# Kernel optimization log

Measured on AMD Instinct MI355X. Metric: run time of the kernel, lower is better.

Reference implementation:

```python
import jax, jax.numpy as jnp
import numpy as np

N = 1000   # node count forced by fc1_1 in_features=1680 (see shape derivation)
E = 8000   # edges, avg degree ~8
F_IN = 6   # node feature dim (first 3 = pos, zeroed in forward)


def setup_inputs() -> dict:
    key = jax.random.key(0)
    ks = jax.random.split(key, 24)
    f = lambda k, s, sc=1.0: jax.random.normal(k, s, dtype=jnp.float32) * sc
    inp = {
        "x": f(ks[0], (N, F_IN)),
        "edge_index": jax.random.randint(ks[1], (2, E), 0, N, dtype=jnp.int64),
        # GCNConv weights (xavier-ish scale)
        "W1": f(ks[2], (F_IN, 32), 0.4), "b1": jnp.zeros((32,), jnp.float32),
        "W2": f(ks[3], (32, 32), 0.18), "b2": jnp.zeros((32,), jnp.float32),
        # Conv2d kernels, OIHW
        "k1": f(ks[4], (3, 1, 3, 2), 0.3), "kb1": jnp.zeros((3,), jnp.float32),
        "k2": f(ks[5], (6, 3, 3, 2), 0.2), "kb2": jnp.zeros((6,), jnp.float32),
        "k3": f(ks[6], (3, 6, 3, 2), 0.2), "kb3": jnp.zeros((3,), jnp.float32),
        "k4": f(ks[7], (1, 3, 3, 2), 0.2), "kb4": jnp.zeros((1,), jnp.float32),
        # FC head (torch Linear layout: [out, in])
        "fw1": f(ks[8], (1024, 1680), 0.02), "fb1": jnp.zeros((1024,), jnp.float32),
        "fw2": f(ks[9], (1024, 1024), 0.03), "fb2": jnp.zeros((1024,), jnp.float32),
        "fw3": f(ks[10], (64, 1024), 0.03), "fb3": jnp.zeros((64,), jnp.float32),
    }
    return inp


def _conv2d(x, w, b):
    out = jax.lax.conv_general_dilated(
        x, w, window_strides=(1, 1), padding="VALID",
        dimension_numbers=("NCHW", "OIHW", "NCHW"))
    return out + b[None, :, None, None]


def _maxpool2(x):  # MaxPool2d((2,1), stride=(2,1))
    return jax.lax.reduce_window(x, -jnp.inf, jax.lax.max,
                                 (1, 1, 2, 1), (1, 1, 2, 1), "VALID")


def reference(x, edge_index, W1, b1, W2, b2, k1, kb1, k2, kb2, k3, kb3, k4, kb4,
              fw1, fb1, fw2, fb2, fw3, fb3):
    num_nodes = x.shape[0]
    # forward zeroes the first 3 features (positions)
    x = x.at[:, :3].set(0.0)

    loop = jnp.arange(num_nodes)
    row = jnp.concatenate([edge_index[0], loop])
    col = jnp.concatenate([edge_index[1], loop])
    deg = jnp.zeros((num_nodes,), x.dtype).at[col].add(1.0)
    dinv = jnp.where(deg > 0, jax.lax.rsqrt(deg), 0.0)
    norm = (dinv[row] * dinv[col])[:, None]  # [E+N, 1]

    def gcn(h, W, b):
        hw = h @ W                                   # [N, 32]
        msg = hw[row] * norm                         # gather + scale
        return jax.ops.segment_sum(msg, col, num_segments=num_nodes) + b

    leaky = lambda v: jnp.where(v > 0, v, 0.2 * v)   # LeakyReLU(0.2)
    h = leaky(gcn(x, W1, b1))
    h = leaky(gcn(h, W2, b2))                        # [N, 32]

    img = h[None, None]                              # [1, 1, N, 32]
    img = _maxpool2(jax.nn.relu(_conv2d(img, k1, kb1)))   # [1,3,499,31]
    img = _maxpool2(jax.nn.relu(_conv2d(img, k2, kb2)))   # [1,6,248,30]
    img = _maxpool2(jax.nn.relu(_conv2d(img, k3, kb3)))   # [1,3,123,29]
    img = _maxpool2(jax.nn.relu(_conv2d(img, k4, kb4)))   # [1,1,60,28]

    v = img.reshape(-1)                              # [1680]
    v = v @ fw1.T + fb1                              # no activation between FCs (as in source)
    v = v @ fw2.T + fb2
    v = v @ fw3.T + fb3                              # [64]
    return v
```

## Files before the change

kernel.cpp:

```cpp
#include <hip/hip_runtime.h>

#define LEAKY(v) ((v) > 0.0f ? (v) : 0.2f * (v))

__global__ void k1_prep(const float* __restrict__ x, const int* __restrict__ col,
                        const float* __restrict__ W1, float* __restrict__ deg,
                        float* __restrict__ aggs ,
                        float* __restrict__ xw, int n, int E) {
    int tid = blockIdx.x * blockDim.x + threadIdx.x;
    int NT = gridDim.x * blockDim.x;
    for (int i = tid; i < 2 * n * 32; i += NT) aggs[i] = 0.0f;
    for (int e = tid; e < E; e += NT) atomicAdd(&deg[col[e]], 1.0f);
    for (int t = tid; t < n * 32; t += NT) {
        int j = t & 31, nn = t >> 5;
        xw[t] = x[nn*6+3] * W1[96+j]
              + x[nn*6+4] * W1[128+j]
              + x[nn*6+5] * W1[160+j];
    }
}

__global__ void k_scatter(const float* __restrict__ xw, const float* __restrict__ deg,
                          const int* __restrict__ row, const int* __restrict__ col,
                          float* __restrict__ agg, int E, int n) {
    int tid = blockIdx.x * blockDim.x + threadIdx.x;
    int total = (E + n) * 32;
    if (tid >= total) return;
    int e = tid >> 5, j = tid & 31;
    int r, c; float nrm;
    if (e < E) {
        r = row[e]; c = col[e];
        nrm = (1.0f / sqrtf(deg[r] + 1.0f)) * (1.0f / sqrtf(deg[c] + 1.0f));
    } else {
        r = c = e - E;
        nrm = 1.0f / (deg[r] + 1.0f);
    }
    atomicAdd(&agg[c * 32 + j], xw[r * 32 + j] * nrm);
}

__global__ void k3_xw2(const float* __restrict__ agg1, const float* __restrict__ b1,
                       const float* __restrict__ W2, float* __restrict__ xw, int n) {
    int tid = blockIdx.x * blockDim.x + threadIdx.x;
    if (tid >= n * 32) return;
    int j = tid & 31, nn = tid >> 5;
    const float* a = agg1 + nn * 32;
    float s = 0.0f;
#pragma unroll
    for (int f = 0; f < 32; ++f) {
        float v = a[f] + b1[f];
        v = LEAKY(v);
        s += v * W2[f * 32 + j];
    }
    xw[tid] = s;
}

__global__ void k5_conv1(const float* __restrict__ h2, const float* __restrict__ b2,
                         const float* __restrict__ w, const float* __restrict__ bias,
                         float* __restrict__ out) {
    const int Hp = 499, Wo = 31, total = 3 * Hp * Wo;
    int t0 = blockIdx.x * blockDim.x + threadIdx.x;
    if (t0 >= total) return;
    int ow = t0 % Wo; int t = t0 / Wo; int oh = t % Hp; int co = t / Hp;
    const float* ip = h2 + (2 * oh) * 32 + ow;
    float vals[4][2];
#pragma unroll
    for (int r = 0; r < 4; ++r)
#pragma unroll
        for (int cx = 0; cx < 2; ++cx) {
            float v = ip[r * 32 + cx] + b2[ow + cx];
            vals[r][cx] = LEAKY(v);
        }
    const float* wp = w + co * 6;
    float a0 = vals[0][0]*wp[0] + vals[0][1]*wp[1] + vals[1][0]*wp[2]
             + vals[1][1]*wp[3] + vals[2][0]*wp[4] + vals[2][1]*wp[5];
    float a1 = vals[1][0]*wp[0] + vals[1][1]*wp[1] + vals[2][0]*wp[2]
             + vals[2][1]*wp[3] + vals[3][0]*wp[4] + vals[3][1]*wp[5];
    float m = fmaxf(a0, a1) + bias[co];
    out[t0] = fmaxf(m, 0.0f);
}

__global__ void k6_conv2(const float* __restrict__ in, const float* __restrict__ w,
                         const float* __restrict__ bias, float* __restrict__ out) {
    const int CI = 3, Hin = 499, Win = 31, Hp = 248, Wo = 30, total = 6 * Hp * Wo;
    int t0 = blockIdx.x * blockDim.x + threadIdx.x;
    if (t0 >= total) return;
    int ow = t0 % Wo; int t = t0 / Wo; int oh = t % Hp; int co = t / Hp;
    float a0 = 0.0f, a1 = 0.0f;
#pragma unroll
    for (int ci = 0; ci < CI; ++ci) {
        const float* q = in + (ci * Hin + 2 * oh) * Win + ow;
        const float* wp = w + (co * CI + ci) * 6;
        float r00 = q[0],     r01 = q[1];
        float r10 = q[Win],   r11 = q[Win+1];
        float r20 = q[2*Win], r21 = q[2*Win+1];
        float r30 = q[3*Win], r31 = q[3*Win+1];
        a0 += r00*wp[0] + r01*wp[1] + r10*wp[2] + r11*wp[3] + r20*wp[4] + r21*wp[5];
        a1 += r10*wp[0] + r11*wp[1] + r20*wp[2] + r21*wp[3] + r30*wp[4] + r31*wp[5];
    }
    float m = fmaxf(a0, a1) + bias[co];
    out[t0] = fmaxf(m, 0.0f);
}

__global__ void k7_conv3(const float* __restrict__ in, const float* __restrict__ w,
                         const float* __restrict__ bias, float* __restrict__ out) {
    const int CI = 6, Hin = 248, Win = 30, Hp = 123, Wo = 29, total = 3 * Hp * Wo;
    int t0 = blockIdx.x * blockDim.x + threadIdx.x;
    if (t0 >= total) return;
    int ow = t0 % Wo; int t = t0 / Wo; int oh = t % Hp; int co = t / Hp;
    float a0 = 0.0f, a1 = 0.0f;
#pragma unroll
    for (int ci = 0; ci < CI; ++ci) {
        const float* q = in + (ci * Hin + 2 * oh) * Win + ow;
        const float* wp = w + (co * CI + ci) * 6;
        float r00 = q[0],     r01 = q[1];
        float r10 = q[Win],   r11 = q[Win+1];
        float r20 = q[2*Win], r21 = q[2*Win+1];
        float r30 = q[3*Win], r31 = q[3*Win+1];
        a0 += r00*wp[0] + r01*wp[1] + r10*wp[2] + r11*wp[3] + r20*wp[4] + r21*wp[5];
        a1 += r10*wp[0] + r11*wp[1] + r20*wp[2] + r21*wp[3] + r30*wp[4] + r31*wp[5];
    }
    float m = fmaxf(a0, a1) + bias[co];
    out[t0] = fmaxf(m, 0.0f);
}

__global__ __launch_bounds__(256) void k8_conv4_fc1(
        const float* __restrict__ c3, const float* __restrict__ k4,
        const float* __restrict__ kb4, const float* __restrict__ fw1,
        const float* __restrict__ fb1, float* __restrict__ f1) {
    __shared__ __align__(16) float lc4[1680];
    const int Hin = 123, Win = 29, Wo = 28;
    float kb = kb4[0];
    for (int t0 = (int)threadIdx.x; t0 < 1680; t0 += 256) {
        int ow = t0 % Wo; int oh = t0 / Wo;
        float a0 = 0.0f, a1 = 0.0f;
#pragma unroll
        for (int ci = 0; ci < 3; ++ci) {
            const float* q = c3 + (ci * Hin + 2 * oh) * Win + ow;
            const float* wp = k4 + ci * 6;
            float r00 = q[0],     r01 = q[1];
            float r10 = q[Win],   r11 = q[Win+1];
            float r20 = q[2*Win], r21 = q[2*Win+1];
            float r30 = q[3*Win], r31 = q[3*Win+1];
            a0 += r00*wp[0] + r01*wp[1] + r10*wp[2] + r11*wp[3] + r20*wp[4] + r21*wp[5];
            a1 += r10*wp[0] + r11*wp[1] + r20*wp[2] + r21*wp[3] + r30*wp[4] + r31*wp[5];
        }
        float m = fmaxf(a0, a1) + kb;
        lc4[t0] = fmaxf(m, 0.0f);
    }
    __syncthreads();
    int wv = threadIdx.x >> 6, lane = threadIdx.x & 63;
    int o = blockIdx.x * 4 + wv;
    const float4* wr = (const float4*)(fw1 + (size_t)o * 1680);
    const float4* vv = (const float4*)lc4;
    float s = 0.0f;
    for (int i = lane; i < 420; i += 64) {
        float4 a = vv[i], ww = wr[i];
        s += a.x*ww.x + a.y*ww.y + a.z*ww.z + a.w*ww.w;
    }
#pragma unroll
    for (int off = 32; off > 0; off >>= 1) s += __shfl_down(s, off, 64);
    if (lane == 0) f1[o] = s + fb1[o];
}

__global__ __launch_bounds__(256) void k_fc1024(const float* __restrict__ v,
                                                const float* __restrict__ w,
                                                const float* __restrict__ b,
                                                float* __restrict__ out) {
    int wv = threadIdx.x >> 6, lane = threadIdx.x & 63;
    int o = blockIdx.x * 4 + wv;
    const float4* wr = (const float4*)(w + (size_t)o * 1024);
    const float4* vv = (const float4*)v;
    float s = 0.0f;
#pragma unroll
    for (int i = 0; i < 4; ++i) {
        float4 a = vv[lane + 64*i], ww = wr[lane + 64*i];
        s += a.x*ww.x + a.y*ww.y + a.z*ww.z + a.w*ww.w;
    }
#pragma unroll
    for (int off = 32; off > 0; off >>= 1) s += __shfl_down(s, off, 64);
    if (lane == 0) out[o] = s + b[o];
}

extern "C" void kernel_launch(void* const* d_in, const int* in_sizes, int n_in,
                              void* d_out, int out_size, void* d_ws, size_t ws_size,
                              hipStream_t stream) {
    const float* x   = (const float*)d_in[0];
    const int*   ei  = (const int*)d_in[1];
    const float* W1  = (const float*)d_in[2];
    const float* b1  = (const float*)d_in[3];
    const float* W2  = (const float*)d_in[4];
    const float* b2  = (const float*)d_in[5];
    const float* k1  = (const float*)d_in[6];
    const float* kb1 = (const float*)d_in[7];
    const float* k2  = (const float*)d_in[8];
    const float* kb2 = (const float*)d_in[9];
    const float* k3  = (const float*)d_in[10];
    const float* kb3 = (const float*)d_in[11];
    const float* k4  = (const float*)d_in[12];
    const float* kb4 = (const float*)d_in[13];
    const float* fw1 = (const float*)d_in[14];
    const float* fb1 = (const float*)d_in[15];
    const float* fw2 = (const float*)d_in[16];
    const float* fb2 = (const float*)d_in[17];
    const float* fw3 = (const float*)d_in[18];
    const float* fb3 = (const float*)d_in[19];

    int n = in_sizes[0] / 6;
    int E = in_sizes[1] / 2;
    const int* row = ei;
    const int* col = ei + E;

    float* ws   = (float*)d_ws;
    float* deg  = ws;
    float* agg1 = ws + 1024;
    float* agg2 = agg1 + 32000;
    float* xw   = agg2 + 32000;
    float* c1   = xw + 32000;
    float* c2   = c1 + 46407;
    float* c3   = c2 + 44640;
    float* f1   = c3 + 10704;
    float* f2   = f1 + 1024;

    const int B = 256;

    hipMemsetAsync(deg, 0, n * sizeof(float), stream);
    k1_prep<<<256, B, 0, stream>>>(x, col, W1, deg, agg1, xw, n, E);
    int st = (E + n) * 32;
    k_scatter<<<(st + B - 1) / B, B, 0, stream>>>(xw, deg, row, col, agg1, E, n);
    k3_xw2<<<(n * 32 + B - 1) / B, B, 0, stream>>>(agg1, b1, W2, xw, n);
    k_scatter<<<(st + B - 1) / B, B, 0, stream>>>(xw, deg, row, col, agg2, E, n);
    k5_conv1<<<(3 * 499 * 31 + B - 1) / B, B, 0, stream>>>(agg2, b2, k1, kb1, c1);
    k6_conv2<<<(6 * 248 * 30 + B - 1) / B, B, 0, stream>>>(c1, k2, kb2, c2);
    k7_conv3<<<(3 * 123 * 29 + B - 1) / B, B, 0, stream>>>(c2, k3, kb3, c3);
    k8_conv4_fc1<<<256, B, 0, stream>>>(c3, k4, kb4, fw1, fb1, f1);
    k_fc1024<<<256, B, 0, stream>>>(f1, fw2, fb2, f2);
    k_fc1024<<<16, B, 0, stream>>>(f2, fw3, fb3, (float*)d_out);
}
```

Measured before the change: 136.0 us.

## Fuse all stages into one cooperative persistent kernel with grid syncs

Replaces the memset plus nine separate kernel launches with a single cooperative kernel of 256 blocks that runs every stage in grid-stride loops, separated by grid.sync barriers. The aim is to remove per-launch overhead and inter-kernel gaps, which likely dominate at this small problem size. In exchange, the scatter and conv stages that previously used many blocks now run on only 256 blocks, and each grid-wide barrier has its own cost. Zeroing of deg and agg buffers also moves inside the kernel.

```diff
diff --git a/kernel.cpp b/kernel.cpp
--- a/kernel.cpp
+++ b/kernel.cpp
@@ -1,236 +1,276 @@
 #include <hip/hip_runtime.h>
+#include <hip/hip_cooperative_groups.h>
+
+namespace cg = cooperative_groups;
 
 #define LEAKY(v) ((v) > 0.0f ? (v) : 0.2f * (v))
 
-__global__ void k1_prep(const float* __restrict__ x, const int* __restrict__ col,
-                        const float* __restrict__ W1, float* __restrict__ deg,
-                        float* __restrict__ aggs ,
-                        float* __restrict__ xw, int n, int E) {
-    int tid = blockIdx.x * blockDim.x + threadIdx.x;
-    int NT = gridDim.x * blockDim.x;
-    for (int i = tid; i < 2 * n * 32; i += NT) aggs[i] = 0.0f;
-    for (int e = tid; e < E; e += NT) atomicAdd(&deg[col[e]], 1.0f);
-    for (int t = tid; t < n * 32; t += NT) {
+struct Params {
+    const float* x;  const int* row; const int* col;
+    const float* W1; const float* b1; const float* W2; const float* b2;
+    const float* k1; const float* kb1; const float* k2; const float* kb2;
+    const float* k3; const float* kb3; const float* k4; const float* kb4;
+    const float* fw1; const float* fb1; const float* fw2; const float* fb2;
+    const float* fw3; const float* fb3;
+    float* deg;
+    float* agg1;
+    float* agg2;
+    float* xw;
+    float* c1;
+    float* c2;
+    float* c3;
+    float* f1;
+    float* f2;
+    float* out;
+    int n; int E;
+};
+
+__global__ __launch_bounds__(256) void fused_all(Params p) {
+    cg::grid_group grid = cg::this_grid();
+    const int T  = blockIdx.x * 256 + (int)threadIdx.x;
+    const int NT = gridDim.x * 256;
+    __shared__ __align__(16) float lc4[1680];
+
+    for (int i = T; i < 1024 + 64000; i += NT) p.deg[i] = 0.0f;
+    grid.sync();
+
+    for (int e = T; e < p.E; e += NT) atomicAdd(&p.deg[p.col[e]], 1.0f);
+    for (int t = T; t < p.n * 32; t += NT) {
         int j = t & 31, nn = t >> 5;
-        xw[t] = x[nn*6+3] * W1[96+j]
-              + x[nn*6+4] * W1[128+j]
-              + x[nn*6+5] * W1[160+j];
-    }
-}
-
-__global__ void k_scatter(const float* __restrict__ xw, const float* __restrict__ deg,
-                          const int* __restrict__ row, const int* __restrict__ col,
-                          float* __restrict__ agg, int E, int n) {
-    int tid = blockIdx.x * blockDim.x + threadIdx.x;
-    int total = (E + n) * 32;
-    if (tid >= total) return;
-    int e = tid >> 5, j = tid & 31;
-    int r, c; float nrm;
-    if (e < E) {
-        r = row[e]; c = col[e];
-        nrm = (1.0f / sqrtf(deg[r] + 1.0f)) * (1.0f / sqrtf(deg[c] + 1.0f));
-    } else {
-        r = c = e - E;
-        nrm = 1.0f / (deg[r] + 1.0f);
-    }
-    atomicAdd(&agg[c * 32 + j], xw[r * 32 + j] * nrm);
-}
-
-__global__ void k3_xw2(const float* __restrict__ agg1, const float* __restrict__ b1,
-                       const float* __restrict__ W2, float* __restrict__ xw, int n) {
-    int tid = blockIdx.x * blockDim.x + threadIdx.x;
-    if (tid >= n * 32) return;
-    int j = tid & 31, nn = tid >> 5;
-    const float* a = agg1 + nn * 32;
-    float s = 0.0f;
-#pragma unroll
-    for (int f = 0; f < 32; ++f) {
-        float v = a[f] + b1[f];
-        v = LEAKY(v);
-        s += v * W2[f * 32 + j];
-    }
-    xw[tid] = s;
-}
-
-__global__ void k5_conv1(const float* __restrict__ h2, const float* __restrict__ b2,
-                         const float* __restrict__ w, const float* __restrict__ bias,
-                         float* __restrict__ out) {
-    const int Hp = 499, Wo = 31, total = 3 * Hp * Wo;
-    int t0 = blockIdx.x * blockDim.x + threadIdx.x;
-    if (t0 >= total) return;
-    int ow = t0 % Wo; int t = t0 / Wo; int oh = t % Hp; int co = t / Hp;
-    const float* ip = h2 + (2 * oh) * 32 + ow;
-    float vals[4][2];
-#pragma unroll
-    for (int r = 0; r < 4; ++r)
-#pragma unroll
-        for (int cx = 0; cx < 2; ++cx) {
-            float v = ip[r * 32 + cx] + b2[ow + cx];
-            vals[r][cx] = LEAKY(v);
-        }
-    const float* wp = w + co * 6;
-    float a0 = vals[0][0]*wp[0] + vals[0][1]*wp[1] + vals[1][0]*wp[2]
-             + vals[1][1]*wp[3] + vals[2][0]*wp[4] + vals[2][1]*wp[5];
-    float a1 = vals[1][0]*wp[0] + vals[1][1]*wp[1] + vals[2][0]*wp[2]
-             + vals[2][1]*wp[3] + vals[3][0]*wp[4] + vals[3][1]*wp[5];
-    float m = fmaxf(a0, a1) + bias[co];
-    out[t0] = fmaxf(m, 0.0f);
-}
-
-__global__ void k6_conv2(const float* __restrict__ in, const float* __restrict__ w,
-                         const float* __restrict__ bias, float* __restrict__ out) {
-    const int CI = 3, Hin = 499, Win = 31, Hp = 248, Wo = 30, total = 6 * Hp * Wo;
-    int t0 = blockIdx.x * blockDim.x + threadIdx.x;
-    if (t0 >= total) return;
-    int ow = t0 % Wo; int t = t0 / Wo; int oh = t % Hp; int co = t / Hp;
-    float a0 = 0.0f, a1 = 0.0f;
-#pragma unroll
-    for (int ci = 0; ci < CI; ++ci) {
-        const float* q = in + (ci * Hin + 2 * oh) * Win + ow;
-        const float* wp = w + (co * CI + ci) * 6;
-        float r00 = q[0],     r01 = q[1];
-        float r10 = q[Win],   r11 = q[Win+1];
-        float r20 = q[2*Win], r21 = q[2*Win+1];
-        float r30 = q[3*Win], r31 = q[3*Win+1];
-        a0 += r00*wp[0] + r01*wp[1] + r10*wp[2] + r11*wp[3] + r20*wp[4] + r21*wp[5];
-        a1 += r10*wp[0] + r11*wp[1] + r20*wp[2] + r21*wp[3] + r30*wp[4] + r31*wp[5];
-    }
-    float m = fmaxf(a0, a1) + bias[co];
-    out[t0] = fmaxf(m, 0.0f);
-}
-
-__global__ void k7_conv3(const float* __restrict__ in, const float* __restrict__ w,
-                         const float* __restrict__ bias, float* __restrict__ out) {
-    const int CI = 6, Hin = 248, Win = 30, Hp = 123, Wo = 29, total = 3 * Hp * Wo;
-    int t0 = blockIdx.x * blockDim.x + threadIdx.x;
-    if (t0 >= total) return;
-    int ow = t0 % Wo; int t = t0 / Wo; int oh = t % Hp; int co = t / Hp;
-    float a0 = 0.0f, a1 = 0.0f;
-#pragma unroll
-    for (int ci = 0; ci < CI; ++ci) {
-        const float* q = in + (ci * Hin + 2 * oh) * Win + ow;
-        const float* wp = w + (co * CI + ci) * 6;
-        float r00 = q[0],     r01 = q[1];
-        float r10 = q[Win],   r11 = q[Win+1];
-        float r20 = q[2*Win], r21 = q[2*Win+1];
-        float r30 = q[3*Win], r31 = q[3*Win+1];
-        a0 += r00*wp[0] + r01*wp[1] + r10*wp[2] + r11*wp[3] + r20*wp[4] + r21*wp[5];
-        a1 += r10*wp[0] + r11*wp[1] + r20*wp[2] + r21*wp[3] + r30*wp[4] + r31*wp[5];
-    }
-    float m = fmaxf(a0, a1) + bias[co];
-    out[t0] = fmaxf(m, 0.0f);
-}
-
-__global__ __launch_bounds__(256) void k8_conv4_fc1(
-        const float* __restrict__ c3, const float* __restrict__ k4,
-        const float* __restrict__ kb4, const float* __restrict__ fw1,
-        const float* __restrict__ fb1, float* __restrict__ f1) {
-    __shared__ __align__(16) float lc4[1680];
-    const int Hin = 123, Win = 29, Wo = 28;
-    float kb = kb4[0];
-    for (int t0 = (int)threadIdx.x; t0 < 1680; t0 += 256) {
-        int ow = t0 % Wo; int oh = t0 / Wo;
-        float a0 = 0.0f, a1 = 0.0f;
-#pragma unroll
-        for (int ci = 0; ci < 3; ++ci) {
-            const float* q = c3 + (ci * Hin + 2 * oh) * Win + ow;
-            const float* wp = k4 + ci * 6;
-            float r00 = q[0],     r01 = q[1];
-            float r10 = q[Win],   r11 = q[Win+1];
-            float r20 = q[2*Win], r21 = q[2*Win+1];
-            float r30 = q[3*Win], r31 = q[3*Win+1];
-            a0 += r00*wp[0] + r01*wp[1] + r10*wp[2] + r11*wp[3] + r20*wp[4] + r21*wp[5];
-            a1 += r10*wp[0] + r11*wp[1] + r20*wp[2] + r21*wp[3] + r30*wp[4] + r31*wp[5];
-        }
-        float m = fmaxf(a0, a1) + kb;
-        lc4[t0] = fmaxf(m, 0.0f);
-    }
-    __syncthreads();
-    int wv = threadIdx.x >> 6, lane = threadIdx.x & 63;
-    int o = blockIdx.x * 4 + wv;
-    const float4* wr = (const float4*)(fw1 + (size_t)o * 1680);
-    const float4* vv = (const float4*)lc4;
-    float s = 0.0f;
-    for (int i = lane; i < 420; i += 64) {
-        float4 a = vv[i], ww = wr[i];
-        s += a.x*ww.x + a.y*ww.y + a.z*ww.z + a.w*ww.w;
-    }
-#pragma unroll
-    for (int off = 32; off > 0; off >>= 1) s += __shfl_down(s, off, 64);
-    if (lane == 0) f1[o] = s + fb1[o];
-}
-
-__global__ __launch_bounds__(256) void k_fc1024(const float* __restrict__ v,
-                                                const float* __restrict__ w,
-                                                const float* __restrict__ b,
-                                                float* __restrict__ out) {
-    int wv = threadIdx.x >> 6, lane = threadIdx.x & 63;
-    int o = blockIdx.x * 4 + wv;
-    const float4* wr = (const float4*)(w + (size_t)o * 1024);
-    const float4* vv = (const float4*)v;
-    float s = 0.0f;
-#pragma unroll
-    for (int i = 0; i < 4; ++i) {
-        float4 a = vv[lane + 64*i], ww = wr[lane + 64*i];
-        s += a.x*ww.x + a.y*ww.y + a.z*ww.z + a.w*ww.w;
-    }
-#pragma unroll
-    for (int off = 32; off > 0; off >>= 1) s += __shfl_down(s, off, 64);
-    if (lane == 0) out[o] = s + b[o];
+        p.xw[t] = p.x[nn*6+3] * p.W1[96+j]
+                + p.x[nn*6+4] * p.W1[128+j]
+                + p.x[nn*6+5] * p.W1[160+j];
+    }
+    grid.sync();
+
+    {
+        const int total = (p.E + p.n) * 32;
+        for (int t = T; t < total; t += NT) {
+            int e = t >> 5, j = t & 31;
+            int r, c; float nrm;
+            if (e < p.E) {
+                r = p.row[e]; c = p.col[e];
+                nrm = (1.0f / sqrtf(p.deg[r] + 1.0f)) * (1.0f / sqrtf(p.deg[c] + 1.0f));
+            } else {
+                r = c = e - p.E;
+                nrm = 1.0f / (p.deg[r] + 1.0f);
+            }
+            atomicAdd(&p.agg1[c * 32 + j], p.xw[r * 32 + j] * nrm);
+        }
+    }
+    grid.sync();
+
+    for (int t = T; t < p.n * 32; t += NT) {
+        int j = t & 31, nn = t >> 5;
+        const float* a = p.agg1 + nn * 32;
+        float s = 0.0f;
+#pragma unroll
+        for (int f = 0; f < 32; ++f) {
+            float v = a[f] + p.b1[f];
+            v = LEAKY(v);
+            s += v * p.W2[f * 32 + j];
+        }
+        p.xw[t] = s;
+    }
+    grid.sync();
+
+    {
+        const int total = (p.E + p.n) * 32;
+        for (int t = T; t < total; t += NT) {
+            int e = t >> 5, j = t & 31;
+            int r, c; float nrm;
+            if (e < p.E) {
+                r = p.row[e]; c = p.col[e];
+                nrm = (1.0f / sqrtf(p.deg[r] + 1.0f)) * (1.0f / sqrtf(p.deg[c] + 1.0f));
+            } else {
+                r = c = e - p.E;
+                nrm = 1.0f / (p.deg[r] + 1.0f);
+            }
+            atomicAdd(&p.agg2[c * 32 + j], p.xw[r * 32 + j] * nrm);
+        }
+    }
+    grid.sync();
+
+    {
+        const int Hp = 499, Wo = 31, total = 3 * Hp * Wo;
+        for (int t0 = T; t0 < total; t0 += NT) {
+            int ow = t0 % Wo; int t = t0 / Wo; int oh = t % Hp; int co = t / Hp;
+            const float* ip = p.agg2 + (2 * oh) * 32 + ow;
+            float vals[4][2];
+#pragma unroll
+            for (int r = 0; r < 4; ++r)
+#pragma unroll
+                for (int cx = 0; cx < 2; ++cx) {
+                    float v = ip[r * 32 + cx] + p.b2[ow + cx];
+                    vals[r][cx] = LEAKY(v);
+                }
+            const float* wp = p.k1 + co * 6;
+            float a0 = vals[0][0]*wp[0] + vals[0][1]*wp[1] + vals[1][0]*wp[2]
+                     + vals[1][1]*wp[3] + vals[2][0]*wp[4] + vals[2][1]*wp[5];
+            float a1 = vals[1][0]*wp[0] + vals[1][1]*wp[1] + vals[2][0]*wp[2]
+                     + vals[2][1]*wp[3] + vals[3][0]*wp[4] + vals[3][1]*wp[5];
+            float m = fmaxf(a0, a1) + p.kb1[co];
+            p.c1[t0] = fmaxf(m, 0.0f);
+        }
+    }
+    grid.sync();
+
+    {
+        const int CI = 3, Hin = 499, Win = 31, Hp = 248, Wo = 30, total = 6 * Hp * Wo;
+        for (int t0 = T; t0 < total; t0 += NT) {
+            int ow = t0 % Wo; int t = t0 / Wo; int oh = t % Hp; int co = t / Hp;
+            float a0 = 0.0f, a1 = 0.0f;
+#pragma unroll
+            for (int ci = 0; ci < CI; ++ci) {
+                const float* q = p.c1 + (ci * Hin + 2 * oh) * Win + ow;
+                const float* wp = p.k2 + (co * CI + ci) * 6;
+                float r00 = q[0],     r01 = q[1];
+                float r10 = q[Win],   r11 = q[Win+1];
+                float r20 = q[2*Win], r21 = q[2*Win+1];
+                float r30 = q[3*Win], r31 = q[3*Win+1];
+                a0 += r00*wp[0] + r01*wp[1] + r10*wp[2] + r11*wp[3] + r20*wp[4] + r21*wp[5];
+                a1 += r10*wp[0] + r11*wp[1] + r20*wp[2] + r21*wp[3] + r30*wp[4] + r31*wp[5];
+            }
+            float m = fmaxf(a0, a1) + p.kb2[co];
+            p.c2[t0] = fmaxf(m, 0.0f);
+        }
+    }
+    grid.sync();
+
+    {
+        const int CI = 6, Hin = 248, Win = 30, Hp = 123, Wo = 29, total = 3 * Hp * Wo;
+        for (int t0 = T; t0 < total; t0 += NT) {
+            int ow = t0 % Wo; int t = t0 / Wo; int oh = t % Hp; int co = t / Hp;
+            float a0 = 0.0f, a1 = 0.0f;
+#pragma unroll
+            for (int ci = 0; ci < CI; ++ci) {
+                const float* q = p.c2 + (ci * Hin + 2 * oh) * Win + ow;
+                const float* wp = p.k3 + (co * CI + ci) * 6;
+                float r00 = q[0],     r01 = q[1];
+                float r10 = q[Win],   r11 = q[Win+1];
+                float r20 = q[2*Win], r21 = q[2*Win+1];
+                float r30 = q[3*Win], r31 = q[3*Win+1];
+                a0 += r00*wp[0] + r01*wp[1] + r10*wp[2] + r11*wp[3] + r20*wp[4] + r21*wp[5];
+                a1 += r10*wp[0] + r11*wp[1] + r20*wp[2] + r21*wp[3] + r30*wp[4] + r31*wp[5];
+            }
+            float m = fmaxf(a0, a1) + p.kb3[co];
+            p.c3[t0] = fmaxf(m, 0.0f);
+        }
+    }
+    grid.sync();
+
+    {
+        const int Hin = 123, Win = 29, Wo = 28;
+        float kb = p.kb4[0];
+        for (int t0 = (int)threadIdx.x; t0 < 1680; t0 += 256) {
+            int ow = t0 % Wo; int oh = t0 / Wo;
+            float a0 = 0.0f, a1 = 0.0f;
+#pragma unroll
+            for (int ci = 0; ci < 3; ++ci) {
+                const float* q = p.c3 + (ci * Hin + 2 * oh) * Win + ow;
+                const float* wp = p.k4 + ci * 6;
+                float r00 = q[0],     r01 = q[1];
+                float r10 = q[Win],   r11 = q[Win+1];
+                float r20 = q[2*Win], r21 = q[2*Win+1];
+                float r30 = q[3*Win], r31 = q[3*Win+1];
+                a0 += r00*wp[0] + r01*wp[1] + r10*wp[2] + r11*wp[3] + r20*wp[4] + r21*wp[5];
+                a1 += r10*wp[0] + r11*wp[1] + r20*wp[2] + r21*wp[3] + r30*wp[4] + r31*wp[5];
+            }
+            float m = fmaxf(a0, a1) + kb;
+            lc4[t0] = fmaxf(m, 0.0f);
+        }
+        __syncthreads();
+        int wv = (int)threadIdx.x >> 6, lane = (int)threadIdx.x & 63;
+        int o = blockIdx.x * 4 + wv;
+        const float4* wr = (const float4*)(p.fw1 + (size_t)o * 1680);
+        const float4* vv = (const float4*)lc4;
+        float s = 0.0f;
+        for (int i = lane; i < 420; i += 64) {
+            float4 a = vv[i], ww = wr[i];
+            s += a.x*ww.x + a.y*ww.y + a.z*ww.z + a.w*ww.w;
+        }
+#pragma unroll
+        for (int off = 32; off > 0; off >>= 1) s += __shfl_down(s, off, 64);
+        if (lane == 0) p.f1[o] = s + p.fb1[o];
+    }
+    grid.sync();
+
+    {
+        int wv = (int)threadIdx.x >> 6, lane = (int)threadIdx.x & 63;
+        int o = blockIdx.x * 4 + wv;
+        const float4* wr = (const float4*)(p.fw2 + (size_t)o * 1024);
+        const float4* vv = (const float4*)p.f1;
+        float s = 0.0f;
+#pragma unroll
+        for (int i = 0; i < 4; ++i) {
+            float4 a = vv[lane + 64*i], ww = wr[lane + 64*i];
+            s += a.x*ww.x + a.y*ww.y + a.z*ww.z + a.w*ww.w;
+        }
+#pragma unroll
+        for (int off = 32; off > 0; off >>= 1) s += __shfl_down(s, off, 64);
+        if (lane == 0) p.f2[o] = s + p.fb2[o];
+    }
+    grid.sync();
+
+    if (blockIdx.x < 16) {
+        int wv = (int)threadIdx.x >> 6, lane = (int)threadIdx.x & 63;
+        int o = blockIdx.x * 4 + wv;
+        const float4* wr = (const float4*)(p.fw3 + (size_t)o * 1024);
+        const float4* vv = (const float4*)p.f2;
+        float s = 0.0f;
+#pragma unroll
+        for (int i = 0; i < 4; ++i) {
+            float4 a = vv[lane + 64*i], ww = wr[lane + 64*i];
+            s += a.x*ww.x + a.y*ww.y + a.z*ww.z + a.w*ww.w;
+        }
+#pragma unroll
+        for (int off = 32; off > 0; off >>= 1) s += __shfl_down(s, off, 64);
+        if (lane == 0) p.out[o] = s + p.fb3[o];
+    }
 }
 
 extern "C" void kernel_launch(void* const* d_in, const int* in_sizes, int n_in,
                               void* d_out, int out_size, void* d_ws, size_t ws_size,
                               hipStream_t stream) {
-    const float* x   = (const float*)d_in[0];
-    const int*   ei  = (const int*)d_in[1];
-    const float* W1  = (const float*)d_in[2];
-    const float* b1  = (const float*)d_in[3];
-    const float* W2  = (const float*)d_in[4];
-    const float* b2  = (const float*)d_in[5];
-    const float* k1  = (const float*)d_in[6];
-    const float* kb1 = (const float*)d_in[7];
-    const float* k2  = (const float*)d_in[8];
-    const float* kb2 = (const float*)d_in[9];
-    const float* k3  = (const float*)d_in[10];
-    const float* kb3 = (const float*)d_in[11];
-    const float* k4  = (const float*)d_in[12];
-    const float* kb4 = (const float*)d_in[13];
-    const float* fw1 = (const float*)d_in[14];
-    const float* fb1 = (const float*)d_in[15];
-    const float* fw2 = (const float*)d_in[16];
-    const float* fb2 = (const float*)d_in[17];
-    const float* fw3 = (const float*)d_in[18];
-    const float* fb3 = (const float*)d_in[19];
-
-    int n = in_sizes[0] / 6;
-    int E = in_sizes[1] / 2;
-    const int* row = ei;
-    const int* col = ei + E;
-
-    float* ws   = (float*)d_ws;
-    float* deg  = ws;
-    float* agg1 = ws + 1024;
-    float* agg2 = agg1 + 32000;
-    float* xw   = agg2 + 32000;
-    float* c1   = xw + 32000;
-    float* c2   = c1 + 46407;
-    float* c3   = c2 + 44640;
-    float* f1   = c3 + 10704;
-    float* f2   = f1 + 1024;
-
-    const int B = 256;
-
-    hipMemsetAsync(deg, 0, n * sizeof(float), stream);
-    k1_prep<<<256, B, 0, stream>>>(x, col, W1, deg, agg1, xw, n, E);
-    int st = (E + n) * 32;
-    k_scatter<<<(st + B - 1) / B, B, 0, stream>>>(xw, deg, row, col, agg1, E, n);
-    k3_xw2<<<(n * 32 + B - 1) / B, B, 0, stream>>>(agg1, b1, W2, xw, n);
-    k_scatter<<<(st + B - 1) / B, B, 0, stream>>>(xw, deg, row, col, agg2, E, n);
-    k5_conv1<<<(3 * 499 * 31 + B - 1) / B, B, 0, stream>>>(agg2, b2, k1, kb1, c1);
-    k6_conv2<<<(6 * 248 * 30 + B - 1) / B, B, 0, stream>>>(c1, k2, kb2, c2);
-    k7_conv3<<<(3 * 123 * 29 + B - 1) / B, B, 0, stream>>>(c2, k3, kb3, c3);
-    k8_conv4_fc1<<<256, B, 0, stream>>>(c3, k4, kb4, fw1, fb1, f1);
-    k_fc1024<<<256, B, 0, stream>>>(f1, fw2, fb2, f2);
-    k_fc1024<<<16, B, 0, stream>>>(f2, fw3, fb3, (float*)d_out);
+    Params hp;
+    hp.x   = (const float*)d_in[0];
+    const int* ei = (const int*)d_in[1];
+    hp.W1  = (const float*)d_in[2];
+    hp.b1  = (const float*)d_in[3];
+    hp.W2  = (const float*)d_in[4];
+    hp.b2  = (const float*)d_in[5];
+    hp.k1  = (const float*)d_in[6];
+    hp.kb1 = (const float*)d_in[7];
+    hp.k2  = (const float*)d_in[8];
+    hp.kb2 = (const float*)d_in[9];
+    hp.k3  = (const float*)d_in[10];
+    hp.kb3 = (const float*)d_in[11];
+    hp.k4  = (const float*)d_in[12];
+    hp.kb4 = (const float*)d_in[13];
+    hp.fw1 = (const float*)d_in[14];
+    hp.fb1 = (const float*)d_in[15];
+    hp.fw2 = (const float*)d_in[16];
+    hp.fb2 = (const float*)d_in[17];
+    hp.fw3 = (const float*)d_in[18];
+    hp.fb3 = (const float*)d_in[19];
+
+    hp.n = in_sizes[0] / 6;
+    hp.E = in_sizes[1] / 2;
+    hp.row = ei;
+    hp.col = ei + hp.E;
+
+    float* ws = (float*)d_ws;
+    hp.deg  = ws;
+    hp.agg1 = ws + 1024;
+    hp.agg2 = hp.agg1 + 32000;
+    hp.xw   = hp.agg2 + 32000;
+    hp.c1   = hp.xw + 32000;
+    hp.c2   = hp.c1 + 46408;
+    hp.c3   = hp.c2 + 44640;
+    hp.f1   = hp.c3 + 10704;
+    hp.f2   = hp.f1 + 1024;
+    hp.out  = (float*)d_out;
+
+    void* args[] = { (void*)&hp };
+    hipLaunchCooperativeKernel((void*)fused_all, dim3(256), dim3(256), args, 0, stream);
 }
```

New measurement: 416.3 us. +206.1%, slower.
